# Performance work log

Measured on AMD Instinct MI355X. Metric: run time of the kernel, lower is better.

The kernel has to match this reference:

```python
import jax, jax.numpy as jnp
import numpy as np

B, A, D = 1024, 200, 128
H = 8
DH = D // H
TANH_CLIP = 10.0


def setup_inputs() -> dict:
    key = jax.random.key(0)
    k = jax.random.split(key, 8)
    agent_embd = jax.random.normal(k[0], (B, A, D), dtype=jnp.float32)
    # old_action must be a permutation per row (no revisits under the mask)
    old_action = jax.vmap(lambda kk: jax.random.permutation(kk, A))(
        jax.random.split(k[1], B)).astype(jnp.int32)
    s = 0.02
    W_placeholder = jax.random.uniform(k[2], (D,), jnp.float32, -1.0, 1.0)
    W_node = jax.random.normal(k[3], (D, 3 * D), jnp.float32) * s   # project_node_embeddings
    W_fixed = jax.random.normal(k[4], (D, D), jnp.float32) * s      # project_fixed_context
    W_step = jax.random.normal(k[5], (D, D), jnp.float32) * s       # project_step_context
    W_out = jax.random.normal(k[6], (D, D), jnp.float32) * s        # project_out
    return {"agent_embd": agent_embd, "old_action": old_action,
            "W_placeholder": W_placeholder, "W_node": W_node,
            "W_fixed": W_fixed, "W_step": W_step, "W_out": W_out}


def _decode(agent_embd, old_action, W_placeholder, W_node, W_fixed, W_step, W_out):
    b_, a_, d_ = agent_embd.shape
    inv_sqrt_dh = np.float32(1.0 / np.sqrt(DH))
    inv_sqrt_d = np.float32(1.0 / np.sqrt(d_))
    batch_ix = jnp.arange(b_)

    # _precompute: fixed context + per-head K/V + logit keys
    graph_embed = agent_embd.mean(axis=1)                      # [B, D]
    fixed_ctx = graph_embed @ W_fixed                          # [B, D]
    proj = agent_embd @ W_node                                 # [B, A, 3D]
    gK, gV, logit_K = jnp.split(proj, 3, axis=-1)              # each [B, A, D]
    gK = gK.reshape(b_, a_, H, DH).transpose(2, 0, 1, 3)       # [H, B, A, dh]
    gV = gV.reshape(b_, a_, H, DH).transpose(2, 0, 1, 3)       # [H, B, A, dh]

    def step(carry, xs):
        mask, prev = carry                                     # [B, A] bool, [B] int
        i, act = xs
        gathered = agent_embd[batch_ix, prev]                  # [B, D]
        step_ctx = jnp.where(i == 0, W_placeholder[None, :], gathered)
        query = fixed_ctx + step_ctx @ W_step                  # [B, D]
        mask = jnp.where(i > 0, mask.at[batch_ix, prev].set(True), mask)

        Q = query.reshape(b_, H, DH).transpose(1, 0, 2)        # [H, B, dh]
        compat = jnp.einsum('hbd,hbad->hba', Q, gK) * inv_sqrt_dh
        compat = jnp.where(mask[None, :, :], -jnp.inf, compat)  # mask_inner
        attn = jax.nn.softmax(compat, axis=-1)                 # [H, B, A]
        heads = jnp.einsum('hba,hbad->hbd', attn, gV)          # [H, B, dh]
        glimpse = heads.transpose(1, 0, 2).reshape(b_, d_) @ W_out  # [B, D]

        logits = jnp.einsum('bd,bad->ba', glimpse, logit_K) * inv_sqrt_d
        logits = jnp.tanh(logits) * TANH_CLIP
        logits = jnp.where(mask, -jnp.inf, logits)             # mask_logits
        log_p = jax.nn.log_softmax(logits, axis=-1)            # [B, A]
        lp_sel = log_p[batch_ix, act]                          # [B]
        return (mask, act), lp_sel

    mask0 = jnp.zeros((b_, a_), dtype=bool)
    prev0 = jnp.zeros((b_,), dtype=old_action.dtype)
    xs = (jnp.arange(a_), old_action.T)
    _, lps = jax.lax.scan(step, (mask0, prev0), xs)            # lps: [A, B]
    return old_action, lps.sum(axis=0)


def reference(agent_embd, old_action, W_placeholder, W_node, W_fixed, W_step, W_out):
    return _decode(agent_embd, old_action, W_placeholder, W_node, W_fixed, W_step, W_out)
```

## Files before the change

### kernel.cpp

```cpp
#include <hip/hip_runtime.h>
#include <cstdint>
#include <cstddef>

#define BB 1024
#define AA 200
#define DD 128
#define HH 8
#define N3 384

typedef unsigned short u16;
typedef unsigned int u32;
typedef __attribute__((ext_vector_type(8))) short bf16x8;
typedef __attribute__((ext_vector_type(4))) float f32x4;

__device__ __forceinline__ float bf2f(u16 v){ return __uint_as_float(((u32)v) << 16); }
__device__ __forceinline__ u16 f2bf(float f){
  u32 u = __float_as_uint(f);
  u32 r = u + 0x7fffu + ((u >> 16) & 1u);
  return (u16)(r >> 16);
}
__device__ __forceinline__ u32 pack2(float lo, float hi){
  return (u32)f2bf(lo) | ((u32)f2bf(hi) << 16);
}
__device__ __forceinline__ bf16x8 pack8(float4 a, float4 b){
  bf16x8 o;
  o[0] = (short)f2bf(a.x); o[1] = (short)f2bf(a.y);
  o[2] = (short)f2bf(a.z); o[3] = (short)f2bf(a.w);
  o[4] = (short)f2bf(b.x); o[5] = (short)f2bf(b.y);
  o[6] = (short)f2bf(b.z); o[7] = (short)f2bf(b.w);
  return o;
}

__global__ void k_act_rank(const int* __restrict__ oa, float* __restrict__ out0,
                           int* __restrict__ rank){
  int m = blockIdx.x * 256 + threadIdx.x;
  if (m >= BB*AA) return;
  int v = oa[m];
  out0[m] = (float)v;
  int b = m / AA;
  int j = m - b*AA;
  rank[b*AA + v] = j;
}

__global__ void k_prep(const float* __restrict__ Wn, const float* __restrict__ Ws,
                       const float* __restrict__ Wo,
                       u16* __restrict__ WnT, u16* __restrict__ WsT,
                       u16* __restrict__ WoT){
  int idx = blockIdx.x * 256 + threadIdx.x;
  if (idx < 49152){
    int n = idx >> 7, k = idx & 127;
    WnT[idx] = f2bf(Wn[k*N3 + n]);
  } else if (idx < 65536){
    int j = idx - 49152;
    int n = j >> 7, k = j & 127;
    WsT[j] = f2bf(Ws[k*DD + n]);
  } else if (idx < 81920){
    int j = idx - 65536;
    int n = j >> 7, k = j & 127;
    WoT[j] = f2bf(Wo[k*DD + n]);
  }
}

__global__ void k_fixed(const float* __restrict__ E, const float* __restrict__ Wf,
                        float* __restrict__ fixedc){
  int b = blockIdx.x;
  int d = threadIdx.x;
  __shared__ float ge[DD];
  const float* Eb = E + (size_t)b*AA*DD;
  float s = 0.f;
  for (int a = 0; a < AA; ++a) s += Eb[a*DD + d];
  ge[d] = s * (1.0f/AA);
  __syncthreads();
  float acc = 0.f;
  for (int k = 0; k < DD; ++k) acc = fmaf(ge[k], Wf[k*DD + d], acc);
  fixedc[b*DD + d] = acc;
}

__global__ __launch_bounds__(256) void k_proj_mfma(const float* __restrict__ E,
                                                   const u16* __restrict__ WnT,
                                                   u16* __restrict__ proj){
  const int t = threadIdx.x;
  const int w = t >> 6, L = t & 63;
  const int l16 = L & 15, lq = L >> 4;
  const int m0 = blockIdx.x * 128;
  const int n0 = blockIdx.y * 128;
  const int row0 = m0 + w*32;

  f32x4 acc[2][8] = {};
  const float* Arow0 = E + (size_t)(row0 + l16)*DD;
  const float* Arow1 = Arow0 + (size_t)16*DD;
  #pragma unroll
  for (int ks = 0; ks < 4; ++ks){
    int ko = ks*32 + lq*8;
    bf16x8 a0 = pack8(*(const float4*)(Arow0 + ko), *(const float4*)(Arow0 + ko + 4));
    bf16x8 a1 = pack8(*(const float4*)(Arow1 + ko), *(const float4*)(Arow1 + ko + 4));
    #pragma unroll
    for (int nt = 0; nt < 8; ++nt){
      union { uint4 u; bf16x8 v; } bb;
      bb.u = *(const uint4*)(WnT + (size_t)(n0 + nt*16 + l16)*DD + ko);
      acc[0][nt] = __builtin_amdgcn_mfma_f32_16x16x32_bf16(a0, bb.v, acc[0][nt], 0, 0, 0);
      acc[1][nt] = __builtin_amdgcn_mfma_f32_16x16x32_bf16(a1, bb.v, acc[1][nt], 0, 0, 0);
    }
  }
  #pragma unroll
  for (int mt = 0; mt < 2; ++mt)
    #pragma unroll
    for (int r = 0; r < 4; ++r){
      int row = row0 + mt*16 + lq*4 + r;
      u16* dst = proj + (size_t)row*N3 + n0;
      #pragma unroll
      for (int nt = 0; nt < 8; ++nt)
        dst[nt*16 + l16] = f2bf(acc[mt][nt][r]);
    }
}

__global__ __launch_bounds__(256) void k_query_mfma(const float* __restrict__ E,
                                                    const int* __restrict__ oa,
                                                    const float* __restrict__ Wp,
                                                    const u16* __restrict__ WsT,
                                                    const float* __restrict__ fixedc,
                                                    u16* __restrict__ qhg){
  const int t = threadIdx.x;
  const int w = t >> 6, L = t & 63;
  const int l16 = L & 15, lq = L >> 4;
  const int m0 = blockIdx.x * 128;
  const int row0 = m0 + w*32;

  const float* src[2];
  #pragma unroll
  for (int mt = 0; mt < 2; ++mt){
    int q = row0 + mt*16 + l16;
    int b = q / AA, i = q - b*AA;
    src[mt] = (i == 0) ? Wp : (E + (size_t)(b*AA + oa[b*AA + i - 1])*DD);
  }

  f32x4 acc[2][8] = {};
  #pragma unroll
  for (int ks = 0; ks < 4; ++ks){
    int ko = ks*32 + lq*8;
    bf16x8 a0 = pack8(*(const float4*)(src[0] + ko), *(const float4*)(src[0] + ko + 4));
    bf16x8 a1 = pack8(*(const float4*)(src[1] + ko), *(const float4*)(src[1] + ko + 4));
    #pragma unroll
    for (int nt = 0; nt < 8; ++nt){
      union { uint4 u; bf16x8 v; } bb;
      bb.u = *(const uint4*)(WsT + (size_t)(nt*16 + l16)*DD + ko);
      acc[0][nt] = __builtin_amdgcn_mfma_f32_16x16x32_bf16(a0, bb.v, acc[0][nt], 0, 0, 0);
      acc[1][nt] = __builtin_amdgcn_mfma_f32_16x16x32_bf16(a1, bb.v, acc[1][nt], 0, 0, 0);
    }
  }
  #pragma unroll
  for (int mt = 0; mt < 2; ++mt)
    #pragma unroll
    for (int r = 0; r < 4; ++r){
      int row = row0 + mt*16 + lq*4 + r;
      int b = row / AA;
      const float* fc = fixedc + (size_t)b*DD;
      u16* dst = qhg + (size_t)row*DD;
      #pragma unroll
      for (int nt = 0; nt < 8; ++nt)
        dst[nt*16 + l16] = f2bf((acc[mt][nt][r] + fc[nt*16 + l16]) * 0.25f);
    }
}

#define KSTR 24
#define VSTR 232
__global__ __launch_bounds__(256) void k_attn(const u16* __restrict__ proj,
                                              const int* __restrict__ rank,
                                              u16* __restrict__ qhg){
  __shared__ __align__(16) u16 KL[208*KSTR];
  __shared__ __align__(16) u16 VT[16*VSTR];
  const int b = blockIdx.x;
  const int h = blockIdx.y;
  const int t = threadIdx.x;
  const int w = t >> 6, L = t & 63;
  const int l16 = L & 15, lq = L >> 4;

  if (t < 192) KL[200*KSTR + t] = 0;
  if (t < 128){ int d = t >> 3, c = t & 7; VT[d*VSTR + 200 + c] = 0; }

  if (t < AA){
    const u16* src = proj + ((size_t)(b*AA + t))*N3 + h*16;
    uint4 k0 = *(const uint4*)(src);
    uint4 k1 = *(const uint4*)(src + 8);
    *(uint4*)&KL[t*KSTR]     = k0;
    *(uint4*)&KL[t*KSTR + 8] = k1;
    const u16* sv = src + 128;
    u16 d16[16];
    *(uint4*)(d16)   = *(const uint4*)(sv);
    *(uint4*)(d16+8) = *(const uint4*)(sv+8);
    #pragma unroll
    for (int d = 0; d < 16; ++d) VT[d*VSTR + t] = d16[d];
  }

  u32 ra_pk[13];
  #pragma unroll
  for (int at = 0; at < 13; ++at){
    int a0 = at*16 + lq*4;
    u32 p = 0;
    if (a0 + 3 < AA){
      int4 rv = *(const int4*)(rank + (size_t)b*AA + a0);
      p = (u32)(rv.x+1) | ((u32)(rv.y+1)<<8) | ((u32)(rv.z+1)<<16) | ((u32)(rv.w+1)<<24);
    }
    ra_pk[at] = p;
  }
  __syncthreads();

  u16* Qbase = qhg + (size_t)b*AA*DD + h*16;
  const float NEG_INF = -__builtin_inff();

  for (int it = w; it < 13; it += 4){
    const int qi = it*16 + l16;
    union { uint4 u; bf16x8 v; } qf8;
    qf8.u.x = 0; qf8.u.y = 0; qf8.u.z = 0; qf8.u.w = 0;
    if (qi < AA){
      uint2 q2 = *(const uint2*)(Qbase + (size_t)qi*DD + lq*4);
      qf8.u.x = q2.x; qf8.u.y = q2.y;
    }

    f32x4 S[13];
    #pragma unroll
    for (int at = 0; at < 13; ++at){
      union { uint4 u; bf16x8 v; } kf8;
      uint2 k2 = *(const uint2*)&KL[(at*16 + l16)*KSTR + lq*4];
      kf8.u.x = k2.x; kf8.u.y = k2.y; kf8.u.z = 0; kf8.u.w = 0;
      f32x4 z = {0.f,0.f,0.f,0.f};
      S[at] = __builtin_amdgcn_mfma_f32_16x16x32_bf16(kf8.v, qf8.v, z, 0, 0, 0);
    }
    const u32 iv = (u32)(qi + 1);
    #pragma unroll
    for (int at = 0; at < 13; ++at){
      const u32 pk = ra_pk[at];
      #pragma unroll
      for (int r = 0; r < 4; ++r)
        if (((pk >> (8*r)) & 0xFFu) < iv) S[at][r] = NEG_INF;
    }
    float mx[13];
    #pragma unroll
    for (int at = 0; at < 13; ++at)
      mx[at] = fmaxf(fmaxf(S[at][0], S[at][1]), fmaxf(S[at][2], S[at][3]));
    float m01 = fmaxf(mx[0], mx[1]),  m23 = fmaxf(mx[2], mx[3]);
    float m45 = fmaxf(mx[4], mx[5]),  m67 = fmaxf(mx[6], mx[7]);
    float m89 = fmaxf(mx[8], mx[9]),  mab = fmaxf(mx[10], mx[11]);
    float m = fmaxf(fmaxf(fmaxf(m01, m23), fmaxf(m45, m67)),
                    fmaxf(fmaxf(m89, mab), mx[12]));
    m = fmaxf(m, __shfl_xor(m, 16));
    m = fmaxf(m, __shfl_xor(m, 32));
    m = fmaxf(m, -1e30f);
    float s0 = 0.f, s1 = 0.f, s2 = 0.f, s3 = 0.f;
    #pragma unroll
    for (int at = 0; at < 13; ++at){
      float e0 = __expf(S[at][0] - m);
      float e1 = __expf(S[at][1] - m);
      float e2 = __expf(S[at][2] - m);
      float e3 = __expf(S[at][3] - m);
      S[at][0] = e0; S[at][1] = e1; S[at][2] = e2; S[at][3] = e3;
      s0 += e0; s1 += e1; s2 += e2; s3 += e3;
    }
    float sum = (s0 + s1) + (s2 + s3);
    sum += __shfl_xor(sum, 16);
    sum += __shfl_xor(sum, 32);
    float inv = 1.0f / sum;
    f32x4 acc = {0.f,0.f,0.f,0.f};
    #pragma unroll
    for (int kt = 0; kt < 13; ++kt){
      union { uint4 u; bf16x8 v; } pa8, vb8;
      pa8.u.x = pack2(S[kt][0], S[kt][1]);
      pa8.u.y = pack2(S[kt][2], S[kt][3]);
      pa8.u.z = 0; pa8.u.w = 0;
      uint2 v2 = *(const uint2*)&VT[l16*VSTR + kt*16 + lq*4];
      vb8.u.x = v2.x; vb8.u.y = v2.y; vb8.u.z = 0; vb8.u.w = 0;
      acc = __builtin_amdgcn_mfma_f32_16x16x32_bf16(vb8.v, pa8.v, acc, 0, 0, 0);
    }
    if (qi < AA){
      uint2 ov;
      ov.x = pack2(acc[0]*inv, acc[1]*inv);
      ov.y = pack2(acc[2]*inv, acc[3]*inv);
      *(uint2*)(Qbase + (size_t)qi*DD + lq*4) = ov;
    }
  }
}

__global__ __launch_bounds__(256) void k_glimpse_mfma(const u16* __restrict__ qhg,
                                                      const u16* __restrict__ WoT,
                                                      u16* __restrict__ proj){
  const int t = threadIdx.x;
  const int w = t >> 6, L = t & 63;
  const int l16 = L & 15, lq = L >> 4;
  const int m0 = blockIdx.x * 128;
  const int row0 = m0 + w*32;

  f32x4 acc[2][8] = {};
  const u16* Arow0 = qhg + (size_t)(row0 + l16)*DD;
  const u16* Arow1 = Arow0 + (size_t)16*DD;
  #pragma unroll
  for (int ks = 0; ks < 4; ++ks){
    int ko = ks*32 + lq*8;
    union { uint4 u; bf16x8 v; } a0, a1;
    a0.u = *(const uint4*)(Arow0 + ko);
    a1.u = *(const uint4*)(Arow1 + ko);
    #pragma unroll
    for (int nt = 0; nt < 8; ++nt){
      union { uint4 u; bf16x8 v; } bb;
      bb.u = *(const uint4*)(WoT + (size_t)(nt*16 + l16)*DD + ko);
      acc[0][nt] = __builtin_amdgcn_mfma_f32_16x16x32_bf16(a0.v, bb.v, acc[0][nt], 0, 0, 0);
      acc[1][nt] = __builtin_amdgcn_mfma_f32_16x16x32_bf16(a1.v, bb.v, acc[1][nt], 0, 0, 0);
    }
  }
  #pragma unroll
  for (int mt = 0; mt < 2; ++mt)
    #pragma unroll
    for (int r = 0; r < 4; ++r){
      int row = row0 + mt*16 + lq*4 + r;
      u16* dst = proj + (size_t)row*N3;
      #pragma unroll
      for (int nt = 0; nt < 8; ++nt)
        dst[nt*16 + l16] = f2bf(acc[mt][nt][r]);
    }
}

__global__ __launch_bounds__(256) void k_logits(const u16* __restrict__ proj,
                                                const int* __restrict__ rank,
                                                const int* __restrict__ oa,
                                                float* __restrict__ outlps){
  __shared__ float red[4];
  const int b = blockIdx.x;
  const int t = threadIdx.x;
  const int w = t >> 6, L = t & 63;
  const int l16 = L & 15, lq = L >> 4;
  const float inv_sqrt_d = 0.08838834764831843f;

  const u16* Gbase  = proj + (size_t)b*AA*N3;
  const u16* LKbase = Gbase + 256;

  int ra[13];
  #pragma unroll
  for (int at = 0; at < 13; ++at){
    int a = at*16 + l16;
    ra[at] = (a < AA) ? rank[b*AA + a] : -1;
  }

  float lp_part = 0.f;

  for (int it = w; it < 13; it += 4){
    bf16x8 af[4];
    {
      const u16* arow = Gbase + (size_t)(it*16 + l16)*N3;
      #pragma unroll
      for (int kb = 0; kb < 4; ++kb){
        union { uint4 u; bf16x8 v; } tmp;
        tmp.u = *(const uint4*)(arow + kb*32 + lq*8);
        af[kb] = tmp.v;
      }
    }
    f32x4 S[13];
    #pragma unroll
    for (int at = 0; at < 13; ++at){
      const u16* brow = LKbase + (size_t)(at*16 + l16)*N3;
      f32x4 acc = {0.f,0.f,0.f,0.f};
      #pragma unroll
      for (int kb = 0; kb < 4; ++kb){
        union { uint4 u; bf16x8 v; } tmp;
        tmp.u = *(const uint4*)(brow + kb*32 + lq*8);
        acc = __builtin_amdgcn_mfma_f32_16x16x32_bf16(af[kb], tmp.v, acc, 0, 0, 0);
      }
      S[at] = acc;
    }
    #pragma unroll
    for (int at = 0; at < 13; ++at)
      #pragma unroll
      for (int r = 0; r < 4; ++r){
        int i = it*16 + lq*4 + r;
        float x = S[at][r] * inv_sqrt_d;
        float e = __expf(2.0f*x);
        float th = 1.0f - 2.0f/(e + 1.0f);
        S[at][r] = (ra[at] < i) ? -__builtin_inff() : 10.0f*th;
      }
    #pragma unroll
    for (int r = 0; r < 4; ++r){
      int i = it*16 + lq*4 + r;
      float m = S[0][r];
      #pragma unroll
      for (int at = 1; at < 13; ++at) m = fmaxf(m, S[at][r]);
      #pragma unroll
      for (int off = 1; off < 16; off <<= 1) m = fmaxf(m, __shfl_xor(m, off));
      float sum = 0.f;
      #pragma unroll
      for (int at = 0; at < 13; ++at) sum += __expf(S[at][r] - m);
      #pragma unroll
      for (int off = 1; off < 16; off <<= 1) sum += __shfl_xor(sum, off);
      if (i < AA){
        float lse = m + __logf(sum);
        int act = oa[b*AA + i];
        if ((act & 15) == l16){
          int at0 = act >> 4;
          #pragma unroll
          for (int at = 0; at < 13; ++at)
            if (at == at0) lp_part += S[at][r] - lse;
        }
      }
    }
  }
  #pragma unroll
  for (int off = 1; off < 64; off <<= 1) lp_part += __shfl_xor(lp_part, off);
  if (L == 0) red[w] = lp_part;
  __syncthreads();
  if (t == 0) outlps[b] = red[0] + red[1] + red[2] + red[3];
}

extern "C" void kernel_launch(void* const* d_in, const int* in_sizes, int n_in,
                              void* d_out, int out_size, void* d_ws, size_t ws_size,
                              hipStream_t stream){
  const float* E  = (const float*)d_in[0];
  const int*   oa = (const int*)d_in[1];
  const float* Wp = (const float*)d_in[2];
  const float* Wn = (const float*)d_in[3];
  const float* Wf = (const float*)d_in[4];
  const float* Ws = (const float*)d_in[5];
  const float* Wo = (const float*)d_in[6];
  float* out = (float*)d_out;

  char* ws = (char*)d_ws;
  int*   rank   = (int*)ws;
  float* fixedc = (float*)(ws + 819200);
  u16*   proj   = (u16*)(ws + 1343488);
  u16*   qhg    = (u16*)(ws + 158629888);
  u16*   WnT    = (u16*)(ws + 211058688);
  u16*   WsT    = (u16*)(ws + 211156992);
  u16*   WoT    = (u16*)(ws + 211189760);

  k_act_rank<<<dim3((BB*AA)/256), 256, 0, stream>>>(oa, out, rank);
  k_prep<<<dim3(320), 256, 0, stream>>>(Wn, Ws, Wo, WnT, WsT, WoT);
  k_fixed<<<dim3(BB), 128, 0, stream>>>(E, Wf, fixedc);
  k_proj_mfma<<<dim3((BB*AA)/128, N3/128), 256, 0, stream>>>(E, WnT, proj);
  k_query_mfma<<<dim3((BB*AA)/128), 256, 0, stream>>>(E, oa, Wp, WsT, fixedc, qhg);
  k_attn<<<dim3(BB, HH), 256, 0, stream>>>(proj, rank, qhg);
  k_glimpse_mfma<<<dim3((BB*AA)/128), 256, 0, stream>>>(qhg, WoT, proj);
  k_logits<<<dim3(BB), 256, 0, stream>>>(proj, rank, oa, out + BB*AA);
}
```

Baseline: 740.8 us.

## Permute keys into action order to make attention mask causal and skip masked tiles

The attention kernel now gathers K/V rows in visit order using old_action, so the per-step mask becomes a simple triangular pattern. Each query tile only processes key tiles from its own diagonal onward, and the rank-based mask loads are removed. Tiles are statically assigned to waves to balance the triangular work, and P is packed to bf16 by truncation instead of rounding. Truncation slightly changes numerics, and the gathered loads are less coalesced.

```diff
diff --git a/kernel.cpp b/kernel.cpp
--- a/kernel.cpp
+++ b/kernel.cpp
@@ -21,6 +21,9 @@
 }
 __device__ __forceinline__ u32 pack2(float lo, float hi){
   return (u32)f2bf(lo) | ((u32)f2bf(hi) << 16);
+}
+__device__ __forceinline__ u32 pack2t(float lo, float hi){
+  return (__float_as_uint(hi) & 0xFFFF0000u) | (__float_as_uint(lo) >> 16);
 }
 __device__ __forceinline__ bf16x8 pack8(float4 a, float4 b){
   bf16x8 o;
@@ -164,8 +167,82 @@
 
 #define KSTR 24
 #define VSTR 232
+template<int IT>
+__device__ __forceinline__ void attn_tile(const u16* KL, const u16* VT,
+                                          u16* Qbase, int l16, int lq,
+                                          bool dm0, bool dm1, bool dm2, bool dm3){
+  constexpr int NT = 13 - IT;
+  const int qi = IT*16 + l16;
+  const float NEG_INF = -__builtin_inff();
+
+  union { uint4 u; bf16x8 v; } qf8;
+  qf8.u.x = 0; qf8.u.y = 0; qf8.u.z = 0; qf8.u.w = 0;
+  if (qi < AA){
+    uint2 q2 = *(const uint2*)(Qbase + (size_t)qi*DD + lq*4);
+    qf8.u.x = q2.x; qf8.u.y = q2.y;
+  }
+
+  f32x4 S[NT];
+  #pragma unroll
+  for (int k = 0; k < NT; ++k){
+    const int at = IT + k;
+    union { uint4 u; bf16x8 v; } kf8;
+    uint2 k2 = *(const uint2*)&KL[(at*16 + l16)*KSTR + lq*4];
+    kf8.u.x = k2.x; kf8.u.y = k2.y; kf8.u.z = 0; kf8.u.w = 0;
+    f32x4 z = {0.f,0.f,0.f,0.f};
+    S[k] = __builtin_amdgcn_mfma_f32_16x16x32_bf16(kf8.v, qf8.v, z, 0, 0, 0);
+  }
+  S[0][0] = dm0 ? NEG_INF : S[0][0];
+  S[0][1] = dm1 ? NEG_INF : S[0][1];
+  S[0][2] = dm2 ? NEG_INF : S[0][2];
+  S[0][3] = dm3 ? NEG_INF : S[0][3];
+  if (lq >= 2){
+    S[NT-1][0] = NEG_INF; S[NT-1][1] = NEG_INF;
+    S[NT-1][2] = NEG_INF; S[NT-1][3] = NEG_INF;
+  }
+  float m = fmaxf(fmaxf(S[0][0], S[0][1]), fmaxf(S[0][2], S[0][3]));
+  #pragma unroll
+  for (int k = 1; k < NT; ++k)
+    m = fmaxf(m, fmaxf(fmaxf(S[k][0], S[k][1]), fmaxf(S[k][2], S[k][3])));
+  m = fmaxf(m, __shfl_xor(m, 16));
+  m = fmaxf(m, __shfl_xor(m, 32));
+  m = fmaxf(m, -1e30f);
+  float s0 = 0.f, s1 = 0.f, s2 = 0.f, s3 = 0.f;
+  #pragma unroll
+  for (int k = 0; k < NT; ++k){
+    float e0 = __expf(S[k][0] - m);
+    float e1 = __expf(S[k][1] - m);
+    float e2 = __expf(S[k][2] - m);
+    float e3 = __expf(S[k][3] - m);
+    S[k][0] = e0; S[k][1] = e1; S[k][2] = e2; S[k][3] = e3;
+    s0 += e0; s1 += e1; s2 += e2; s3 += e3;
+  }
+  float sum = (s0 + s1) + (s2 + s3);
+  sum += __shfl_xor(sum, 16);
+  sum += __shfl_xor(sum, 32);
+  float inv = 1.0f / sum;
+  f32x4 acc = {0.f,0.f,0.f,0.f};
+  #pragma unroll
+  for (int k = 0; k < NT; ++k){
+    const int at = IT + k;
+    union { uint4 u; bf16x8 v; } pa8, vb8;
+    pa8.u.x = pack2t(S[k][0], S[k][1]);
+    pa8.u.y = pack2t(S[k][2], S[k][3]);
+    pa8.u.z = 0; pa8.u.w = 0;
+    uint2 v2 = *(const uint2*)&VT[l16*VSTR + at*16 + lq*4];
+    vb8.u.x = v2.x; vb8.u.y = v2.y; vb8.u.z = 0; vb8.u.w = 0;
+    acc = __builtin_amdgcn_mfma_f32_16x16x32_bf16(vb8.v, pa8.v, acc, 0, 0, 0);
+  }
+  if (qi < AA){
+    uint2 ov;
+    ov.x = pack2(acc[0]*inv, acc[1]*inv);
+    ov.y = pack2(acc[2]*inv, acc[3]*inv);
+    *(uint2*)(Qbase + (size_t)qi*DD + lq*4) = ov;
+  }
+}
+
 __global__ __launch_bounds__(256) void k_attn(const u16* __restrict__ proj,
-                                              const int* __restrict__ rank,
+                                              const int* __restrict__ oa,
                                               u16* __restrict__ qhg){
   __shared__ __align__(16) u16 KL[208*KSTR];
   __shared__ __align__(16) u16 VT[16*VSTR];
@@ -179,7 +256,8 @@
   if (t < 128){ int d = t >> 3, c = t & 7; VT[d*VSTR + 200 + c] = 0; }
 
   if (t < AA){
-    const u16* src = proj + ((size_t)(b*AA + t))*N3 + h*16;
+    int a = oa[(size_t)b*AA + t];
+    const u16* src = proj + ((size_t)(b*AA + a))*N3 + h*16;
     uint4 k0 = *(const uint4*)(src);
     uint4 k1 = *(const uint4*)(src + 8);
     *(uint4*)&KL[t*KSTR]     = k0;
@@ -191,92 +269,31 @@
     #pragma unroll
     for (int d = 0; d < 16; ++d) VT[d*VSTR + t] = d16[d];
   }
-
-  u32 ra_pk[13];
-  #pragma unroll
-  for (int at = 0; at < 13; ++at){
-    int a0 = at*16 + lq*4;
-    u32 p = 0;
-    if (a0 + 3 < AA){
-      int4 rv = *(const int4*)(rank + (size_t)b*AA + a0);
-      p = (u32)(rv.x+1) | ((u32)(rv.y+1)<<8) | ((u32)(rv.z+1)<<16) | ((u32)(rv.w+1)<<24);
-    }
-    ra_pk[at] = p;
-  }
   __syncthreads();
 
   u16* Qbase = qhg + (size_t)b*AA*DD + h*16;
-  const float NEG_INF = -__builtin_inff();
-
-  for (int it = w; it < 13; it += 4){
-    const int qi = it*16 + l16;
-    union { uint4 u; bf16x8 v; } qf8;
-    qf8.u.x = 0; qf8.u.y = 0; qf8.u.z = 0; qf8.u.w = 0;
-    if (qi < AA){
-      uint2 q2 = *(const uint2*)(Qbase + (size_t)qi*DD + lq*4);
-      qf8.u.x = q2.x; qf8.u.y = q2.y;
-    }
-
-    f32x4 S[13];
-    #pragma unroll
-    for (int at = 0; at < 13; ++at){
-      union { uint4 u; bf16x8 v; } kf8;
-      uint2 k2 = *(const uint2*)&KL[(at*16 + l16)*KSTR + lq*4];
-      kf8.u.x = k2.x; kf8.u.y = k2.y; kf8.u.z = 0; kf8.u.w = 0;
-      f32x4 z = {0.f,0.f,0.f,0.f};
-      S[at] = __builtin_amdgcn_mfma_f32_16x16x32_bf16(kf8.v, qf8.v, z, 0, 0, 0);
-    }
-    const u32 iv = (u32)(qi + 1);
-    #pragma unroll
-    for (int at = 0; at < 13; ++at){
-      const u32 pk = ra_pk[at];
-      #pragma unroll
-      for (int r = 0; r < 4; ++r)
-        if (((pk >> (8*r)) & 0xFFu) < iv) S[at][r] = NEG_INF;
-    }
-    float mx[13];
-    #pragma unroll
-    for (int at = 0; at < 13; ++at)
-      mx[at] = fmaxf(fmaxf(S[at][0], S[at][1]), fmaxf(S[at][2], S[at][3]));
-    float m01 = fmaxf(mx[0], mx[1]),  m23 = fmaxf(mx[2], mx[3]);
-    float m45 = fmaxf(mx[4], mx[5]),  m67 = fmaxf(mx[6], mx[7]);
-    float m89 = fmaxf(mx[8], mx[9]),  mab = fmaxf(mx[10], mx[11]);
-    float m = fmaxf(fmaxf(fmaxf(m01, m23), fmaxf(m45, m67)),
-                    fmaxf(fmaxf(m89, mab), mx[12]));
-    m = fmaxf(m, __shfl_xor(m, 16));
-    m = fmaxf(m, __shfl_xor(m, 32));
-    m = fmaxf(m, -1e30f);
-    float s0 = 0.f, s1 = 0.f, s2 = 0.f, s3 = 0.f;
-    #pragma unroll
-    for (int at = 0; at < 13; ++at){
-      float e0 = __expf(S[at][0] - m);
-      float e1 = __expf(S[at][1] - m);
-      float e2 = __expf(S[at][2] - m);
-      float e3 = __expf(S[at][3] - m);
-      S[at][0] = e0; S[at][1] = e1; S[at][2] = e2; S[at][3] = e3;
-      s0 += e0; s1 += e1; s2 += e2; s3 += e3;
-    }
-    float sum = (s0 + s1) + (s2 + s3);
-    sum += __shfl_xor(sum, 16);
-    sum += __shfl_xor(sum, 32);
-    float inv = 1.0f / sum;
-    f32x4 acc = {0.f,0.f,0.f,0.f};
-    #pragma unroll
-    for (int kt = 0; kt < 13; ++kt){
-      union { uint4 u; bf16x8 v; } pa8, vb8;
-      pa8.u.x = pack2(S[kt][0], S[kt][1]);
-      pa8.u.y = pack2(S[kt][2], S[kt][3]);
-      pa8.u.z = 0; pa8.u.w = 0;
-      uint2 v2 = *(const uint2*)&VT[l16*VSTR + kt*16 + lq*4];
-      vb8.u.x = v2.x; vb8.u.y = v2.y; vb8.u.z = 0; vb8.u.w = 0;
-      acc = __builtin_amdgcn_mfma_f32_16x16x32_bf16(vb8.v, pa8.v, acc, 0, 0, 0);
-    }
-    if (qi < AA){
-      uint2 ov;
-      ov.x = pack2(acc[0]*inv, acc[1]*inv);
-      ov.y = pack2(acc[2]*inv, acc[3]*inv);
-      *(uint2*)(Qbase + (size_t)qi*DD + lq*4) = ov;
-    }
+  const bool dm0 = (lq*4 + 0) < l16;
+  const bool dm1 = (lq*4 + 1) < l16;
+  const bool dm2 = (lq*4 + 2) < l16;
+  const bool dm3 = (lq*4 + 3) < l16;
+
+  if (w == 0){
+    attn_tile<0>(KL, VT, Qbase, l16, lq, dm0, dm1, dm2, dm3);
+    attn_tile<3>(KL, VT, Qbase, l16, lq, dm0, dm1, dm2, dm3);
+  } else if (w == 1){
+    attn_tile<1>(KL, VT, Qbase, l16, lq, dm0, dm1, dm2, dm3);
+    attn_tile<2>(KL, VT, Qbase, l16, lq, dm0, dm1, dm2, dm3);
+  } else if (w == 2){
+    attn_tile<4>(KL, VT, Qbase, l16, lq, dm0, dm1, dm2, dm3);
+    attn_tile<6>(KL, VT, Qbase, l16, lq, dm0, dm1, dm2, dm3);
+    attn_tile<8>(KL, VT, Qbase, l16, lq, dm0, dm1, dm2, dm3);
+    attn_tile<10>(KL, VT, Qbase, l16, lq, dm0, dm1, dm2, dm3);
+    attn_tile<12>(KL, VT, Qbase, l16, lq, dm0, dm1, dm2, dm3);
+  } else {
+    attn_tile<5>(KL, VT, Qbase, l16, lq, dm0, dm1, dm2, dm3);
+    attn_tile<7>(KL, VT, Qbase, l16, lq, dm0, dm1, dm2, dm3);
+    attn_tile<9>(KL, VT, Qbase, l16, lq, dm0, dm1, dm2, dm3);
+    attn_tile<11>(KL, VT, Qbase, l16, lq, dm0, dm1, dm2, dm3);
   }
 }
 
@@ -433,7 +450,7 @@
   k_fixed<<<dim3(BB), 128, 0, stream>>>(E, Wf, fixedc);
   k_proj_mfma<<<dim3((BB*AA)/128, N3/128), 256, 0, stream>>>(E, WnT, proj);
   k_query_mfma<<<dim3((BB*AA)/128), 256, 0, stream>>>(E, oa, Wp, WsT, fixedc, qhg);
-  k_attn<<<dim3(BB, HH), 256, 0, stream>>>(proj, rank, qhg);
+  k_attn<<<dim3(BB, HH), 256, 0, stream>>>(proj, oa, qhg);
   k_glimpse_mfma<<<dim3((BB*AA)/128), 256, 0, stream>>>(qhg, WoT, proj);
   k_logits<<<dim3(BB), 256, 0, stream>>>(proj, rank, oa, out + BB*AA);
 }
```

New measurement: 649.1 us. 12.4% less time.
